# Performance work log

Hardware: AMD Instinct MI355X
Metric: run time of the kernel (lower is better)

Reference implementation:

```python
import jax, jax.numpy as jnp
import numpy as np

N_NODES = 50000
N_EDGES = 600000
N_GRAPHS = 64
D_FEAT = 128
DIM_H = 128
N_HOPS = 3
OUT_DIM = 10


def setup_inputs() -> dict:
    key = jax.random.key(0)
    ks = jax.random.split(key, 16)
    x = jax.random.normal(ks[0], (N_NODES, D_FEAT), dtype=jnp.float32)
    edge_index = jax.random.randint(ks[1], (2, N_EDGES), 0, N_NODES, dtype=jnp.int64)
    batch = jnp.sort(jax.random.randint(ks[2], (N_NODES,), 0, N_GRAPHS, dtype=jnp.int64))
    def glorot(k, shape):
        fan = shape[0] + shape[1]
        return jax.random.uniform(k, shape, jnp.float32, -1.0, 1.0) * np.sqrt(6.0 / fan)
    # GCNConv weights stored as [in, out]; Linear weights stored as [in, out]
    W1 = glorot(ks[3], (D_FEAT, DIM_H)); b1 = jnp.zeros((DIM_H,), jnp.float32)
    W2 = glorot(ks[4], (DIM_H, DIM_H)); b2 = jnp.zeros((DIM_H,), jnp.float32)
    W3 = glorot(ks[5], (DIM_H, DIM_H)); b3 = jnp.zeros((DIM_H,), jnp.float32)
    H3 = DIM_H * N_HOPS
    lin1_W = glorot(ks[6], (H3, H3)); lin1_b = jnp.zeros((H3,), jnp.float32)
    lin2_W = glorot(ks[7], (H3, OUT_DIM)); lin2_b = jnp.zeros((OUT_DIM,), jnp.float32)
    return {"x": x, "W1": W1, "b1": b1, "W2": W2, "b2": b2, "W3": W3, "b3": b3,
            "lin1_W": lin1_W, "lin1_b": lin1_b, "lin2_W": lin2_W, "lin2_b": lin2_b,
            "edge_index": edge_index, "batch": batch}


def gcn_conv(x, W, b, src, dst, n_nodes):
    # PyG GCNConv (add_self_loops=True, normalize=True):
    #   deg[i] = in-degree at target + 1 (self loop); norm = d^-1/2[src] * d^-1/2[dst]
    deg = jnp.zeros((n_nodes,), x.dtype).at[dst].add(1.0) + 1.0
    dinv = jax.lax.rsqrt(deg)
    xw = x @ W  # [N, H] transform before propagate
    coef = (dinv[src] * dinv[dst])[:, None]
    agg = jnp.zeros_like(xw).at[dst].add(xw[src] * coef)
    agg = agg + xw * (dinv * dinv)[:, None]  # self-loop messages
    return agg + b


def global_mean_pool(h, batch, n_graphs):
    sums = jax.ops.segment_sum(h, batch, num_segments=n_graphs)
    cnt = jax.ops.segment_sum(jnp.ones((h.shape[0],), h.dtype), batch, num_segments=n_graphs)
    return sums / jnp.maximum(cnt, 1.0)[:, None]


def reference(x, W1, b1, W2, b2, W3, b3, lin1_W, lin1_b, lin2_W, lin2_b, edge_index, batch):
    src, dst = edge_index[0], edge_index[1]
    n = x.shape[0]
    h1 = gcn_conv(x, W1, b1, src, dst, n)
    h2 = gcn_conv(h1, W2, b2, src, dst, n)
    h3 = gcn_conv(h2, W3, b3, src, dst, n)
    pooled = jnp.concatenate([global_mean_pool(h, batch, N_GRAPHS) for h in (h1, h2, h3)], axis=1)
    h = jax.nn.relu(pooled @ lin1_W + lin1_b)
    # dropout is identity in eval mode
    h = h @ lin2_W + lin2_b
    return (h, jax.nn.log_softmax(h, axis=1))
```

## Files before the change

kernel.cpp:

```cpp
#include <hip/hip_runtime.h>
#include <hip/hip_fp16.h>
#include <math.h>

#define N_NODES 50000
#define N_EDGES 600000
#define N_GRAPHS 64
#define DFEAT 128
#define H3 384
#define OUTD 10
#define SCAN_BLOCKS 196
#define FILL_BLOCKS 2344
#define POOL_CHUNKS 16
#define APAD 136

typedef _Float16 f16x8 __attribute__((ext_vector_type(8)));
typedef float f32x4 __attribute__((ext_vector_type(4)));
typedef float f32x2 __attribute__((ext_vector_type(2)));

__global__ __launch_bounds__(256) void k_deg(const int* __restrict__ ei, int* __restrict__ deg,
                                             int* __restrict__ rank) {
    int e = blockIdx.x * 256 + threadIdx.x;
    if (e >= N_EDGES) return;
    int dst = ei[N_EDGES + e];
    rank[e] = atomicAdd(&deg[dst], 1);
}

__global__ __launch_bounds__(256) void k_part(const int* __restrict__ deg, int* __restrict__ part) {
    __shared__ int red[256];
    int tid = threadIdx.x;
    int i = blockIdx.x * 256 + tid;
    red[tid] = (i < N_NODES) ? deg[i] : 0;
    __syncthreads();
    for (int s = 128; s > 0; s >>= 1) {
        if (tid < s) red[tid] += red[tid + s];
        __syncthreads();
    }
    if (tid == 0) part[blockIdx.x] = red[0];
}

__global__ __launch_bounds__(256) void k_offsets(const int* __restrict__ deg, const int* __restrict__ part,
                                                 int* __restrict__ offs, float* __restrict__ dinv) {
    __shared__ int pbuf[256];
    __shared__ int buf[256];
    int tid = threadIdx.x;
    int pv = (tid < SCAN_BLOCKS) ? part[tid] : 0;
    pbuf[tid] = pv;
    __syncthreads();
    for (int d = 1; d < 256; d <<= 1) {
        int t = (tid >= d) ? pbuf[tid - d] : 0;
        __syncthreads();
        pbuf[tid] += t;
        __syncthreads();
    }
    int base = (blockIdx.x > 0) ? pbuf[blockIdx.x - 1] : 0;
    int i = blockIdx.x * 256 + tid;
    int v = (i < N_NODES) ? deg[i] : 0;
    buf[tid] = v;
    __syncthreads();
    for (int d = 1; d < 256; d <<= 1) {
        int t = (tid >= d) ? buf[tid - d] : 0;
        __syncthreads();
        buf[tid] += t;
        __syncthreads();
    }
    if (i < N_NODES) {
        int excl = base + buf[tid] - v;
        offs[i] = excl;
        dinv[i] = rsqrtf((float)v + 1.0f);
        if (i == N_NODES - 1) offs[N_NODES] = base + buf[tid];
    }
}

__global__ __launch_bounds__(256) void k_fill_prep(const int* __restrict__ ei, const int* __restrict__ offs,
                                                   const int* __restrict__ rank, const float* __restrict__ dinv,
                                                   unsigned int* __restrict__ epack,
                                                   const float* __restrict__ W1, const float* __restrict__ W2,
                                                   const float* __restrict__ W3, _Float16* __restrict__ Wt,
                                                   float* __restrict__ pooled) {
    int b = blockIdx.x;
    if (b < FILL_BLOCKS) {
        int e = b * 256 + threadIdx.x;
        if (e >= N_EDGES) return;
        int s = ei[e];
        int t = ei[N_EDGES + e];
        unsigned short dh = __half_as_ushort(__float2half(dinv[s]));
        epack[offs[t] + rank[e]] = (unsigned int)s | ((unsigned int)dh << 16);
    } else if (b < FILL_BLOCKS + 192) {
        int idx = (b - FILL_BLOCKS) * 256 + threadIdx.x;
        int l = idx >> 14, r = idx & 16383;
        const float* W = (l == 0) ? W1 : (l == 1) ? W2 : W3;
        int k = r >> 7, n = r & 127;
        Wt[l * 16384 + n * 128 + k] = (_Float16)W[k * 128 + n];
    } else {
        int idx = (b - FILL_BLOCKS - 192) * 256 + threadIdx.x;
        if (idx < N_GRAPHS * H3) pooled[idx] = 0.0f;
    }
}

template <bool A_FP16>
__global__ __launch_bounds__(256) void gemm_mfma(const void* __restrict__ Aptr, const _Float16* __restrict__ Wt,
                                                 unsigned char* __restrict__ T, int M) {
    __shared__ _Float16 Ws[128 * APAD];
    int tid = threadIdx.x;
    int base = blockIdx.x * 64;
    for (int c = tid; c < 2048; c += 256) {
        int n = c >> 4, c8 = (c & 15) << 3;
        *(f16x8*)&Ws[n * APAD + c8] = *(const f16x8*)&Wt[n * 128 + c8];
    }
    int wave = tid >> 6, lane = tid & 63;
    int m = lane & 15, quad = lane >> 4;
    int gr = base + wave * 16 + m;
    int grc = (gr < M) ? gr : (M - 1);
    f16x8 areg[4];
    if (A_FP16) {
        const _Float16* A = (const _Float16*)Aptr;
#pragma unroll
        for (int kc = 0; kc < 4; ++kc)
            areg[kc] = *(const f16x8*)&A[(size_t)grc * 128 + kc * 32 + quad * 8];
    } else {
        const float* A = (const float*)Aptr;
#pragma unroll
        for (int kc = 0; kc < 4; ++kc) {
            const float* src = A + (size_t)grc * 128 + kc * 32 + quad * 8;
            float4 v0 = *(const float4*)(src);
            float4 v1 = *(const float4*)(src + 4);
            f16x8 h;
            h[0] = (_Float16)v0.x; h[1] = (_Float16)v0.y; h[2] = (_Float16)v0.z; h[3] = (_Float16)v0.w;
            h[4] = (_Float16)v1.x; h[5] = (_Float16)v1.y; h[6] = (_Float16)v1.z; h[7] = (_Float16)v1.w;
            areg[kc] = h;
        }
    }
    __syncthreads();
    f32x4 acc[8];
#pragma unroll
    for (int ct = 0; ct < 8; ++ct) acc[ct] = (f32x4){0.f, 0.f, 0.f, 0.f};
#pragma unroll
    for (int kc = 0; kc < 4; ++kc) {
#pragma unroll
        for (int ct = 0; ct < 8; ++ct) {
            f16x8 b = *(const f16x8*)&Ws[(ct * 16 + m) * APAD + kc * 32 + quad * 8];
            acc[ct] = __builtin_amdgcn_mfma_f32_16x16x32_f16(b, areg[kc], acc[ct], 0, 0, 0);
        }
    }
    if (gr < M) {
#pragma unroll
        for (int ct = 0; ct < 8; ++ct) {
            int col = ct * 16 + quad * 4;
            int p = __builtin_amdgcn_cvt_pk_fp8_f32(acc[ct][0], acc[ct][1], 0, false);
            p     = __builtin_amdgcn_cvt_pk_fp8_f32(acc[ct][2], acc[ct][3], p, true);
            *(int*)(T + (size_t)gr * 128 + col) = p;
        }
    }
}

__global__ __launch_bounds__(256) void gather_agg(const unsigned short* __restrict__ T16,
                                                  const unsigned int* __restrict__ epack,
                                                  const int* __restrict__ offs,
                                                  const float* __restrict__ dinv, const float* __restrict__ bias,
                                                  __half2* __restrict__ H2) {
    int w = threadIdx.x >> 6;
    int l64 = threadIdx.x & 63;
    int node = blockIdx.x * 4 + w;
    unsigned su = T16[(size_t)node * 64 + l64];
    float di = dinv[node];
    float2 b2 = *(const float2*)(bias + l64 * 2);
    float a0 = 0.f, a1 = 0.f;
    int lo = offs[node], hi = offs[node + 1];
    int hm1 = hi - 1;
    for (int e0 = lo; e0 < hi; e0 += 16) {
        unsigned p[16];
#pragma unroll
        for (int j = 0; j < 16; ++j) p[j] = epack[min(e0 + j, hm1)];
        unsigned u[16];
#pragma unroll
        for (int j = 0; j < 16; ++j) u[j] = T16[(size_t)(p[j] & 0xffffu) * 64 + l64];
#pragma unroll
        for (int j = 0; j < 16; ++j) {
            float c = (e0 + j < hi) ? __half2float(__ushort_as_half((unsigned short)(p[j] >> 16))) : 0.0f;
            f32x2 tl = __builtin_amdgcn_cvt_pk_f32_fp8(u[j], false);
            a0 += tl.x * c; a1 += tl.y * c;
        }
    }
    f32x2 sl = __builtin_amdgcn_cvt_pk_f32_fp8(su, false);
    float dd = di * di;
    float r0 = di * a0 + sl.x * dd + b2.x;
    float r1 = di * a1 + sl.y * dd + b2.y;
    H2[(size_t)node * 64 + l64] = __floats2half2_rn(r0, r1);
}

__global__ __launch_bounds__(256) void pool_kernel(const __half2* __restrict__ H0,
                                                   const __half2* __restrict__ H1,
                                                   const __half2* __restrict__ H2buf,
                                                   const int* __restrict__ batch,
                                                   float* __restrict__ pooled) {
    __shared__ int bounds[2];
    __shared__ float2 red[256];
    int g = blockIdx.x >> 4;
    int chunk = blockIdx.x & (POOL_CHUNKS - 1);
    int tid = threadIdx.x;
    int d2 = tid & 63, sub = tid >> 6;
    if (tid < 2) {
        int target = g + tid;
        int lo = 0, hi = N_NODES;
        while (lo < hi) {
            int mid = (lo + hi) >> 1;
            if (batch[mid] < target) lo = mid + 1; else hi = mid;
        }
        bounds[tid] = lo;
    }
    __syncthreads();
    int lo = bounds[0], hi = bounds[1];
    int n = hi - lo;
    int per = (n + POOL_CHUNKS - 1) / POOL_CHUNKS;
    int s = lo + chunk * per;
    int e = s + per; if (e > hi) e = hi;
    const __half2* Hs[3] = {H0, H1, H2buf};
    for (int l = 0; l < 3; ++l) {
        const __half2* H = Hs[l];
        float ax = 0.0f, ay = 0.0f;
        for (int r = s + sub; r < e; r += 4) {
            float2 v = __half22float2(H[(size_t)r * 64 + d2]);
            ax += v.x; ay += v.y;
        }
        red[tid] = make_float2(ax, ay);
        __syncthreads();
        if (sub == 0 && s < e) {
            float2 v0 = red[d2], v1 = red[64 + d2], v2 = red[128 + d2], v3 = red[192 + d2];
            atomicAdd(&pooled[g * H3 + l * 128 + d2 * 2],     v0.x + v1.x + v2.x + v3.x);
            atomicAdd(&pooled[g * H3 + l * 128 + d2 * 2 + 1], v0.y + v1.y + v2.y + v3.y);
        }
        __syncthreads();
    }
}

__global__ __launch_bounds__(384) void mlp_kernel(const float* __restrict__ pooled,
                                                  const int* __restrict__ batch,
                                                  const float* __restrict__ l1W, const float* __restrict__ l1b,
                                                  const float* __restrict__ l2W, const float* __restrict__ l2b,
                                                  float* __restrict__ out) {
    __shared__ float p[H3];
    __shared__ float hid[H3];
    __shared__ float o10[OUTD];
    __shared__ int bnd[2];
    int g = blockIdx.x, tid = threadIdx.x;
    if (tid < 2) {
        int target = g + tid;
        int lo = 0, hi = N_NODES;
        while (lo < hi) {
            int mid = (lo + hi) >> 1;
            if (batch[mid] < target) lo = mid + 1; else hi = mid;
        }
        bnd[tid] = lo;
    }
    __syncthreads();
    float inv = 1.0f / fmaxf((float)(bnd[1] - bnd[0]), 1.0f);
    p[tid] = pooled[g * H3 + tid] * inv;
    __syncthreads();
    float acc = l1b[tid];
    for (int k = 0; k < H3; ++k) acc += p[k] * l1W[k * H3 + tid];
    hid[tid] = fmaxf(acc, 0.0f);
    __syncthreads();
    if (tid < OUTD) {
        float o = l2b[tid];
        for (int k = 0; k < H3; ++k) o += hid[k] * l2W[k * OUTD + tid];
        o10[tid] = o;
        out[g * OUTD + tid] = o;
    }
    __syncthreads();
    if (tid == 0) {
        float m = o10[0];
        for (int j = 1; j < OUTD; ++j) m = fmaxf(m, o10[j]);
        float s = 0.0f;
        for (int j = 0; j < OUTD; ++j) s += expf(o10[j] - m);
        float lse = m + logf(s);
        for (int j = 0; j < OUTD; ++j) out[N_GRAPHS * OUTD + g * OUTD + j] = o10[j] - lse;
    }
}

extern "C" void kernel_launch(void* const* d_in, const int* in_sizes, int n_in,
                              void* d_out, int out_size, void* d_ws, size_t ws_size,
                              hipStream_t stream) {
    const float* x      = (const float*)d_in[0];
    const float* W1     = (const float*)d_in[1];
    const float* b1     = (const float*)d_in[2];
    const float* W2     = (const float*)d_in[3];
    const float* b2     = (const float*)d_in[4];
    const float* W3     = (const float*)d_in[5];
    const float* b3     = (const float*)d_in[6];
    const float* lin1_W = (const float*)d_in[7];
    const float* lin1_b = (const float*)d_in[8];
    const float* lin2_W = (const float*)d_in[9];
    const float* lin2_b = (const float*)d_in[10];
    const int* edge_index = (const int*)d_in[11];
    const int* batch      = (const int*)d_in[12];

    char* ws = (char*)d_ws;
    auto alloc = [&](size_t bytes) -> void* {
        void* p = (void*)ws;
        ws += (bytes + 255) & ~(size_t)255;
        return p;
    };
    int*   deg    = (int*)  alloc((size_t)N_NODES * 4);
    int*   part   = (int*)  alloc((size_t)SCAN_BLOCKS * 4);
    int*   offs   = (int*)  alloc((size_t)(N_NODES + 1) * 4);
    int*   rank   = (int*)  alloc((size_t)N_EDGES * 4);
    float* dinv   = (float*)alloc((size_t)N_NODES * 4);
    unsigned int* epack = (unsigned int*)alloc((size_t)N_EDGES * 4);
    unsigned char* T = (unsigned char*)alloc((size_t)N_NODES * 128);
    __half* Hbuf[3];
    for (int l = 0; l < 3; ++l) Hbuf[l] = (__half*)alloc((size_t)N_NODES * 128 * 2);
    _Float16* Wt  = (_Float16*)alloc((size_t)3 * 128 * 128 * 2);
    float* pooled = (float*)alloc((size_t)N_GRAPHS * H3 * 4);

    hipMemsetAsync(deg, 0, (size_t)N_NODES * 4, stream);
    k_deg<<<(N_EDGES + 255) / 256, 256, 0, stream>>>(edge_index, deg, rank);
    k_part<<<SCAN_BLOCKS, 256, 0, stream>>>(deg, part);
    k_offsets<<<SCAN_BLOCKS, 256, 0, stream>>>(deg, part, offs, dinv);
    k_fill_prep<<<FILL_BLOCKS + 192 + 96, 256, 0, stream>>>(edge_index, offs, rank, dinv, epack,
                                                            W1, W2, W3, Wt, pooled);

    const float* bs[3] = {b1, b2, b3};
    for (int l = 0; l < 3; ++l) {
        if (l == 0)
            gemm_mfma<false><<<(N_NODES + 63) / 64, 256, 0, stream>>>(x, Wt, T, N_NODES);
        else
            gemm_mfma<true><<<(N_NODES + 63) / 64, 256, 0, stream>>>(Hbuf[l - 1], Wt + (size_t)l * 16384, T, N_NODES);
        gather_agg<<<N_NODES / 4, 256, 0, stream>>>((const unsigned short*)T, epack, offs, dinv, bs[l], (__half2*)Hbuf[l]);
    }
    pool_kernel<<<N_GRAPHS * POOL_CHUNKS, 256, 0, stream>>>((const __half2*)Hbuf[0], (const __half2*)Hbuf[1],
                                                            (const __half2*)Hbuf[2], batch, pooled);
    mlp_kernel<<<N_GRAPHS, 384, 0, stream>>>(pooled, batch, lin1_W, lin1_b, lin2_W, lin2_b, (float*)d_out);
}
```

Before: 293.5 us.

## Gather fp8 rows with 16-byte loads, four edges per half-wave

Restructures the CSR gather-aggregate kernel so each node is handled by 32 lanes instead of 64. Eight lanes each load 16 bytes of an fp8 row, and four edges are processed in parallel per half-wave. Partial sums are combined with xor shuffles and each lane writes four fp16 outputs. This cuts the number of memory instructions per gathered row and raises bytes per load, at the cost of more registers, shuffle reductions and wasted lanes for low-degree nodes.

```diff
diff --git a/kernel.cpp b/kernel.cpp
--- a/kernel.cpp
+++ b/kernel.cpp
@@ -153,39 +153,66 @@
     }
 }
 
-__global__ __launch_bounds__(256) void gather_agg(const unsigned short* __restrict__ T16,
+__global__ __launch_bounds__(256) void gather_agg(const unsigned int* __restrict__ T32,
                                                   const unsigned int* __restrict__ epack,
                                                   const int* __restrict__ offs,
                                                   const float* __restrict__ dinv, const float* __restrict__ bias,
                                                   __half2* __restrict__ H2) {
-    int w = threadIdx.x >> 6;
-    int l64 = threadIdx.x & 63;
-    int node = blockIdx.x * 4 + w;
-    unsigned su = T16[(size_t)node * 64 + l64];
+    const uint4* T128 = (const uint4*)T32;
+    int h = threadIdx.x >> 5;
+    int l32 = threadIdx.x & 31;
+    int e4 = l32 >> 3;
+    int d8 = l32 & 7;
+    int node = blockIdx.x * 8 + h;
     float di = dinv[node];
-    float2 b2 = *(const float2*)(bias + l64 * 2);
-    float a0 = 0.f, a1 = 0.f;
     int lo = offs[node], hi = offs[node + 1];
     int hm1 = hi - 1;
+    float acc[16];
+#pragma unroll
+    for (int k = 0; k < 16; ++k) acc[k] = 0.f;
     for (int e0 = lo; e0 < hi; e0 += 16) {
-        unsigned p[16];
-#pragma unroll
-        for (int j = 0; j < 16; ++j) p[j] = epack[min(e0 + j, hm1)];
-        unsigned u[16];
-#pragma unroll
-        for (int j = 0; j < 16; ++j) u[j] = T16[(size_t)(p[j] & 0xffffu) * 64 + l64];
-#pragma unroll
-        for (int j = 0; j < 16; ++j) {
-            float c = (e0 + j < hi) ? __half2float(__ushort_as_half((unsigned short)(p[j] >> 16))) : 0.0f;
-            f32x2 tl = __builtin_amdgcn_cvt_pk_f32_fp8(u[j], false);
-            a0 += tl.x * c; a1 += tl.y * c;
-        }
-    }
-    f32x2 sl = __builtin_amdgcn_cvt_pk_f32_fp8(su, false);
+        unsigned p[4];
+#pragma unroll
+        for (int b = 0; b < 4; ++b) p[b] = epack[min(e0 + b * 4 + e4, hm1)];
+        uint4 u[4];
+#pragma unroll
+        for (int b = 0; b < 4; ++b) u[b] = T128[(size_t)(p[b] & 0xffffu) * 8 + d8];
+#pragma unroll
+        for (int b = 0; b < 4; ++b) {
+            float c = (e0 + b * 4 + e4 < hi) ? __half2float(__ushort_as_half((unsigned short)(p[b] >> 16))) : 0.0f;
+            f32x2 v0 = __builtin_amdgcn_cvt_pk_f32_fp8(u[b].x, false);
+            f32x2 v1 = __builtin_amdgcn_cvt_pk_f32_fp8(u[b].x, true);
+            f32x2 v2 = __builtin_amdgcn_cvt_pk_f32_fp8(u[b].y, false);
+            f32x2 v3 = __builtin_amdgcn_cvt_pk_f32_fp8(u[b].y, true);
+            f32x2 v4 = __builtin_amdgcn_cvt_pk_f32_fp8(u[b].z, false);
+            f32x2 v5 = __builtin_amdgcn_cvt_pk_f32_fp8(u[b].z, true);
+            f32x2 v6 = __builtin_amdgcn_cvt_pk_f32_fp8(u[b].w, false);
+            f32x2 v7 = __builtin_amdgcn_cvt_pk_f32_fp8(u[b].w, true);
+            acc[0]  += v0.x * c; acc[1]  += v0.y * c; acc[2]  += v1.x * c; acc[3]  += v1.y * c;
+            acc[4]  += v2.x * c; acc[5]  += v2.y * c; acc[6]  += v3.x * c; acc[7]  += v3.y * c;
+            acc[8]  += v4.x * c; acc[9]  += v4.y * c; acc[10] += v5.x * c; acc[11] += v5.y * c;
+            acc[12] += v6.x * c; acc[13] += v6.y * c; acc[14] += v7.x * c; acc[15] += v7.y * c;
+        }
+    }
+#pragma unroll
+    for (int k = 0; k < 16; ++k) {
+        acc[k] += __shfl_xor(acc[k], 8);
+        acc[k] += __shfl_xor(acc[k], 16);
+    }
+    unsigned sudw = T32[(size_t)node * 32 + d8 * 4 + e4];
+    float4 b4 = *(const float4*)(bias + d8 * 16 + e4 * 4);
+    f32x2 sl = __builtin_amdgcn_cvt_pk_f32_fp8(sudw, false);
+    f32x2 sh = __builtin_amdgcn_cvt_pk_f32_fp8(sudw, true);
     float dd = di * di;
-    float r0 = di * a0 + sl.x * dd + b2.x;
-    float r1 = di * a1 + sl.y * dd + b2.y;
-    H2[(size_t)node * 64 + l64] = __floats2half2_rn(r0, r1);
+    int k0 = e4 * 4;
+    float r0 = di * acc[k0 + 0] + sl.x * dd + b4.x;
+    float r1 = di * acc[k0 + 1] + sl.y * dd + b4.y;
+    float r2 = di * acc[k0 + 2] + sh.x * dd + b4.z;
+    float r3 = di * acc[k0 + 3] + sh.y * dd + b4.w;
+    __half2 ha = __floats2half2_rn(r0, r1);
+    __half2 hb = __floats2half2_rn(r2, r3);
+    uint2 st = make_uint2(*(unsigned*)&ha, *(unsigned*)&hb);
+    *(uint2*)&H2[(size_t)node * 64 + d8 * 8 + e4 * 2] = st;
 }
 
 __global__ __launch_bounds__(256) void pool_kernel(const __half2* __restrict__ H0,
@@ -325,7 +352,7 @@
             gemm_mfma<false><<<(N_NODES + 63) / 64, 256, 0, stream>>>(x, Wt, T, N_NODES);
         else
             gemm_mfma<true><<<(N_NODES + 63) / 64, 256, 0, stream>>>(Hbuf[l - 1], Wt + (size_t)l * 16384, T, N_NODES);
-        gather_agg<<<N_NODES / 4, 256, 0, stream>>>((const unsigned short*)T, epack, offs, dinv, bs[l], (__half2*)Hbuf[l]);
+        gather_agg<<<N_NODES / 8, 256, 0, stream>>>((const unsigned int*)T, epack, offs, dinv, bs[l], (__half2*)Hbuf[l]);
     }
     pool_kernel<<<N_GRAPHS * POOL_CHUNKS, 256, 0, stream>>>((const __half2*)Hbuf[0], (const __half2*)Hbuf[1],
                                                             (const __half2*)Hbuf[2], batch, pooled);
```

New measurement: 282.5 us. 1.04x faster.

## Split gather aggregation into feature halves with 16 lanes per node

Applied to the files above, without the earlier changes.

The aggregation kernel now assigns 16 lanes per node, each reading a 4-byte word (four fp8 features), and splits the 128 features into two halves handled by separate blocks. Each wave covers four nodes instead of one, so divergence from uneven degree is spread differently and each lane issues wider gather loads. The cost is that edge metadata is loaded twice (once per half) and each lane does twice the conversion work. The output is written as 8-byte stores.

```diff
diff --git a/kernel.cpp b/kernel.cpp
--- a/kernel.cpp
+++ b/kernel.cpp
@@ -12,6 +12,7 @@
 #define FILL_BLOCKS 2344
 #define POOL_CHUNKS 16
 #define APAD 136
+#define GHALF 3125
 
 typedef _Float16 f16x8 __attribute__((ext_vector_type(8)));
 typedef float f32x4 __attribute__((ext_vector_type(4)));
@@ -153,18 +154,22 @@
     }
 }
 
-__global__ __launch_bounds__(256) void gather_agg(const unsigned short* __restrict__ T16,
+__global__ __launch_bounds__(256) void gather_agg(const unsigned int* __restrict__ T32,
                                                   const unsigned int* __restrict__ epack,
                                                   const int* __restrict__ offs,
                                                   const float* __restrict__ dinv, const float* __restrict__ bias,
                                                   __half2* __restrict__ H2) {
-    int w = threadIdx.x >> 6;
-    int l64 = threadIdx.x & 63;
-    int node = blockIdx.x * 4 + w;
-    unsigned su = T16[(size_t)node * 64 + l64];
+    int b = blockIdx.x;
+    int half = (b >= GHALF) ? 1 : 0;
+    int nb = b - half * GHALF;
+    int q = threadIdx.x >> 4;
+    int l16 = threadIdx.x & 15;
+    int node = nb * 16 + q;
+    int cbase = half * 16 + l16;
+    unsigned su = T32[(size_t)node * 32 + cbase];
     float di = dinv[node];
-    float2 b2 = *(const float2*)(bias + l64 * 2);
-    float a0 = 0.f, a1 = 0.f;
+    float4 b4 = *(const float4*)(bias + half * 64 + l16 * 4);
+    float a0 = 0.f, a1 = 0.f, a2 = 0.f, a3 = 0.f;
     int lo = offs[node], hi = offs[node + 1];
     int hm1 = hi - 1;
     for (int e0 = lo; e0 < hi; e0 += 16) {
@@ -173,19 +178,25 @@
         for (int j = 0; j < 16; ++j) p[j] = epack[min(e0 + j, hm1)];
         unsigned u[16];
 #pragma unroll
-        for (int j = 0; j < 16; ++j) u[j] = T16[(size_t)(p[j] & 0xffffu) * 64 + l64];
+        for (int j = 0; j < 16; ++j) u[j] = T32[(size_t)(p[j] & 0xffffu) * 32 + cbase];
 #pragma unroll
         for (int j = 0; j < 16; ++j) {
             float c = (e0 + j < hi) ? __half2float(__ushort_as_half((unsigned short)(p[j] >> 16))) : 0.0f;
             f32x2 tl = __builtin_amdgcn_cvt_pk_f32_fp8(u[j], false);
-            a0 += tl.x * c; a1 += tl.y * c;
-        }
-    }
-    f32x2 sl = __builtin_amdgcn_cvt_pk_f32_fp8(su, false);
+            f32x2 th = __builtin_amdgcn_cvt_pk_f32_fp8(u[j], true);
+            a0 += tl.x * c; a1 += tl.y * c; a2 += th.x * c; a3 += th.y * c;
+        }
+    }
+    f32x2 sl = __builtin_amdgcn_cvt_pk_f32_fp8(su, false), sh = __builtin_amdgcn_cvt_pk_f32_fp8(su, true);
     float dd = di * di;
-    float r0 = di * a0 + sl.x * dd + b2.x;
-    float r1 = di * a1 + sl.y * dd + b2.y;
-    H2[(size_t)node * 64 + l64] = __floats2half2_rn(r0, r1);
+    float r0 = di * a0 + sl.x * dd + b4.x;
+    float r1 = di * a1 + sl.y * dd + b4.y;
+    float r2 = di * a2 + sh.x * dd + b4.z;
+    float r3 = di * a3 + sh.y * dd + b4.w;
+    __half2 ha = __floats2half2_rn(r0, r1);
+    __half2 hb = __floats2half2_rn(r2, r3);
+    uint2 st = make_uint2(*(unsigned*)&ha, *(unsigned*)&hb);
+    *(uint2*)&H2[(size_t)node * 64 + half * 32 + l16 * 2] = st;
 }
 
 __global__ __launch_bounds__(256) void pool_kernel(const __half2* __restrict__ H0,
@@ -325,7 +336,7 @@
             gemm_mfma<false><<<(N_NODES + 63) / 64, 256, 0, stream>>>(x, Wt, T, N_NODES);
         else
             gemm_mfma<true><<<(N_NODES + 63) / 64, 256, 0, stream>>>(Hbuf[l - 1], Wt + (size_t)l * 16384, T, N_NODES);
-        gather_agg<<<N_NODES / 4, 256, 0, stream>>>((const unsigned short*)T, epack, offs, dinv, bs[l], (__half2*)Hbuf[l]);
+        gather_agg<<<2 * GHALF, 256, 0, stream>>>((const unsigned int*)T, epack, offs, dinv, bs[l], (__half2*)Hbuf[l]);
     }
     pool_kernel<<<N_GRAPHS * POOL_CHUNKS, 256, 0, stream>>>((const __half2*)Hbuf[0], (const __half2*)Hbuf[1],
                                                             (const __half2*)Hbuf[2], batch, pooled);
```

Measured after the change: 275.3 us. 6.2% less time.
